# Optimization experiments

Hardware: AMD Instinct MI355X
Metric: run time of the kernel (lower is better)

Reference implementation:

```python
import jax, jax.numpy as jnp
import numpy as np

N = 100000   # nodes
E = 1600000  # edges (avg degree 16)
F = 128      # input features
H = 64       # hidden_dim
C = 10       # num_classes
G = 128      # graphs in batch
EPS = 1e-5   # BatchNorm eps


def setup_inputs() -> dict:
    key = jax.random.key(0)
    ks = jax.random.split(key, 24)
    d = {}
    d['x'] = jax.random.normal(ks[0], (N, F), jnp.float32)
    d['edge_index'] = jax.random.randint(ks[1], (2, E), 0, N)
    d['batch'] = jnp.sort(jax.random.randint(ks[2], (N,), 0, G))
    # SAGEConv1: lin_l (aggregated, with bias) + lin_r (root, no bias)
    d['W1l'] = jax.random.normal(ks[3], (F, H), jnp.float32) * 0.05
    d['W1r'] = jax.random.normal(ks[4], (F, H), jnp.float32) * 0.05
    d['b1'] = jnp.zeros((H,), jnp.float32)
    # SAGEConv2
    d['W2l'] = jax.random.normal(ks[5], (H, H), jnp.float32) * 0.1
    d['W2r'] = jax.random.normal(ks[6], (H, H), jnp.float32) * 0.1
    d['b2'] = jnp.zeros((H,), jnp.float32)
    # BatchNorm (eval mode: running stats)
    for i, (kg, kb, km, kv) in enumerate([(7, 8, 9, 10), (11, 12, 13, 14), (15, 16, 17, 18)], 1):
        d[f'bn{i}_g'] = jax.random.uniform(ks[kg], (H,), jnp.float32, 0.5, 1.5)
        d[f'bn{i}_b'] = jax.random.normal(ks[kb], (H,), jnp.float32) * 0.1
        d[f'bn{i}_m'] = jax.random.normal(ks[km], (H,), jnp.float32) * 0.1
        d[f'bn{i}_v'] = jax.random.uniform(ks[kv], (H,), jnp.float32, 0.5, 1.5)
    # classifier head
    d['Wc1'] = jax.random.normal(ks[19], (H, H), jnp.float32) * 0.1
    d['bc1'] = jnp.zeros((H,), jnp.float32)
    d['Wc2'] = jax.random.normal(ks[20], (H, C), jnp.float32) * 0.1
    d['bc2'] = jnp.zeros((C,), jnp.float32)
    return d


def _bn(x, g, b, m, v):
    return (x - m) * jax.lax.rsqrt(v + EPS) * g + b


def _sage(x, src, dst, Wl, Wr, b):
    # mean aggregation of source-node features at destination nodes
    msum = jax.ops.segment_sum(x[src], dst, num_segments=N)          # [N, d]
    cnt = jax.ops.segment_sum(jnp.ones((E,), x.dtype), dst, num_segments=N)
    mean = msum / jnp.maximum(cnt, 1.0)[:, None]
    return mean @ Wl + b + x @ Wr


def reference(x, edge_index, batch,
              W1l, W1r, b1, W2l, W2r, b2,
              bn1_g, bn1_b, bn1_m, bn1_v,
              bn2_g, bn2_b, bn2_m, bn2_v,
              Wc1, bc1, bn3_g, bn3_b, bn3_m, bn3_v,
              Wc2, bc2):
    src, dst = edge_index[0], edge_index[1]
    h = _sage(x, src, dst, W1l, W1r, b1)
    h = jax.nn.relu(_bn(h, bn1_g, bn1_b, bn1_m, bn1_v))
    h = _sage(h, src, dst, W2l, W2r, b2)
    h = jax.nn.relu(_bn(h, bn2_g, bn2_b, bn2_m, bn2_v))
    # global mean pool over graphs
    gsum = jax.ops.segment_sum(h, batch, num_segments=G)             # [G, H]
    gcnt = jax.ops.segment_sum(jnp.ones((N,), h.dtype), batch, num_segments=G)
    g = gsum / jnp.maximum(gcnt, 1.0)[:, None]
    # classifier head (eval: dropout is identity)
    g = jax.nn.relu(_bn(g @ Wc1 + bc1, bn3_g, bn3_b, bn3_m, bn3_v))
    logits = g @ Wc2 + bc2
    return jax.nn.log_softmax(logits, axis=1)
```

## Files before the change

### kernel.cpp

```cpp
#include <hip/hip_runtime.h>
#include <hip/hip_bf16.h>
#include <math.h>

#define NN 100000
#define NE 1600000
#define FF 128
#define HH 64
#define CC 10
#define GG 128
#define BN_EPS 1e-5f

#define BNODES 64
#define NB 1563
#define PBLK 128
#define ECHUNK 12500
#define MHIST (NB * PBLK)
#define NSCAN 782
#define SCOL_CAP 2048

typedef short v8bf __attribute__((ext_vector_type(8)));
typedef float v4f  __attribute__((ext_vector_type(4)));

__device__ inline ushort f2b(float x) {
    __hip_bfloat16 h = __float2bfloat16(x);
    return *reinterpret_cast<ushort*>(&h);
}
__device__ inline float b2f(ushort u) {
    return __uint_as_float(((unsigned)u) << 16);
}
__device__ inline float blo(unsigned u) { return __uint_as_float(u << 16); }
__device__ inline float bhi(unsigned u) { return __uint_as_float(u & 0xffff0000u); }

__device__ inline void acc8(float* a, const uint4 r) {
    a[0] += blo(r.x); a[1] += bhi(r.x); a[2] += blo(r.y); a[3] += bhi(r.y);
    a[4] += blo(r.z); a[5] += bhi(r.z); a[6] += blo(r.w); a[7] += bhi(r.w);
}

__device__ inline void sw_one(const float* __restrict__ W, ushort* __restrict__ o,
                              int t, int K) {
    const int lane = t & 63, nt = (t >> 6) & 3, ks = t >> 8;
    const int m = lane & 15, quad = lane >> 4;
#pragma unroll
    for (int j = 0; j < 8; ++j) {
        const int kk = ks * 32 + quad * 8 + j;
        const int cc = nt * 16 + m;
        o[t * 8 + j] = f2b(W[kk * 64 + cc]);
    }
}

template<int K, int TPB, bool AF32>
__global__ __launch_bounds__(256) void gemm_mfma(const void* __restrict__ Xv,
                                                 const ushort* __restrict__ Bl,
                                                 const ushort* __restrict__ Br,
                                                 ushort* __restrict__ Yl,
                                                 ushort* __restrict__ Yr) {
    constexpr int KS = K / 32;
    const int lane  = threadIdx.x & 63;
    const int wave  = threadIdx.x >> 6;
    const int nhalf = wave & 1;
    const int rsub  = wave >> 1;
    const int m = lane & 15, quad = lane >> 4;

    v8bf bl[KS][2], br[KS][2];
#pragma unroll
    for (int ks = 0; ks < KS; ++ks)
#pragma unroll
        for (int nt = 0; nt < 2; ++nt) {
            const int nti = nhalf * 2 + nt;
            bl[ks][nt] = *(const v8bf*)(Bl + ((size_t)(ks * 4 + nti) * 64 + lane) * 8);
            br[ks][nt] = *(const v8bf*)(Br + ((size_t)(ks * 4 + nti) * 64 + lane) * 8);
        }

    for (int it = 0; it < TPB; ++it) {
        const int bt = blockIdx.x * TPB + it;
        const int row0 = bt * 32 + rsub * 16;
        if (row0 >= NN) return;
        const v4f z = {0.f, 0.f, 0.f, 0.f};
        v4f accl[2] = {z, z}, accr[2] = {z, z};
#pragma unroll
        for (int ks = 0; ks < KS; ++ks) {
            v8bf a;
            if (AF32) {
                const float* xrow = (const float*)Xv + (size_t)(row0 + m) * K + quad * 8 + ks * 32;
                const float4 a0 = *(const float4*)(xrow);
                const float4 a1 = *(const float4*)(xrow + 4);
                a[0] = (short)f2b(a0.x); a[1] = (short)f2b(a0.y);
                a[2] = (short)f2b(a0.z); a[3] = (short)f2b(a0.w);
                a[4] = (short)f2b(a1.x); a[5] = (short)f2b(a1.y);
                a[6] = (short)f2b(a1.z); a[7] = (short)f2b(a1.w);
            } else {
                const ushort* xrow = (const ushort*)Xv + (size_t)(row0 + m) * K + quad * 8 + ks * 32;
                a = *(const v8bf*)xrow;
            }
#pragma unroll
            for (int nt = 0; nt < 2; ++nt) {
                accl[nt] = __builtin_amdgcn_mfma_f32_16x16x32_bf16(a, bl[ks][nt], accl[nt], 0, 0, 0);
                accr[nt] = __builtin_amdgcn_mfma_f32_16x16x32_bf16(a, br[ks][nt], accr[nt], 0, 0, 0);
            }
        }
#pragma unroll
        for (int nt = 0; nt < 2; ++nt) {
            const int cc = nhalf * 32 + nt * 16 + m;
#pragma unroll
            for (int r = 0; r < 4; ++r) {
                const size_t off = (size_t)(row0 + quad * 4 + r) * 64 + cc;
                Yl[off] = f2b(accl[nt][r]);
                Yr[off] = f2b(accr[nt][r]);
            }
        }
    }
}

__global__ __launch_bounds__(1024) void edge_hist(const int* __restrict__ dst,
                                                  int* __restrict__ hist,
                                                  const float* __restrict__ W1l,
                                                  const float* __restrict__ W1r,
                                                  const float* __restrict__ W2l,
                                                  const float* __restrict__ W2r,
                                                  ushort* __restrict__ w1ls,
                                                  ushort* __restrict__ w1rs,
                                                  ushort* __restrict__ w2ls,
                                                  ushort* __restrict__ w2rs,
                                                  float* __restrict__ gz) {
    if (blockIdx.x >= PBLK) {
        const int t = threadIdx.x;
        if (blockIdx.x == PBLK) {
            sw_one(W1l, w1ls, t, FF);
            sw_one(W1r, w1rs, t, FF);
        } else {
            if (t < 512) {
                sw_one(W2l, w2ls, t, HH);
                sw_one(W2r, w2rs, t, HH);
            } else {
                for (int i = t - 512; i < GG * 64 + GG; i += 512) gz[i] = 0.f;
            }
        }
        return;
    }
    __shared__ int h[NB];
    for (int i = threadIdx.x; i < NB; i += 1024) h[i] = 0;
    __syncthreads();
    const int e0 = blockIdx.x * ECHUNK;
    for (int e = e0 + threadIdx.x; e < e0 + ECHUNK; e += 1024)
        atomicAdd(&h[dst[e] >> 6], 1);
    __syncthreads();
    for (int i = threadIdx.x; i < NB; i += 1024)
        hist[i * PBLK + blockIdx.x] = h[i];
}

__global__ __launch_bounds__(256) void scan_block(const int* __restrict__ cnt,
                                                  int* __restrict__ rp,
                                                  int* __restrict__ bsum) {
    __shared__ int ws[4];
    const int tid = threadIdx.x;
    const int lane = tid & 63, wv = tid >> 6;
    const int i = blockIdx.x * 256 + tid;
    const int v = (i < MHIST) ? cnt[i] : 0;
    int inc = v;
#pragma unroll
    for (int off = 1; off < 64; off <<= 1) {
        int t = __shfl_up(inc, off, 64);
        if (lane >= off) inc += t;
    }
    if (lane == 63) ws[wv] = inc;
    __syncthreads();
    int wbase = 0;
#pragma unroll
    for (int w = 0; w < 4; ++w) wbase += (w < wv) ? ws[w] : 0;
    if (i < MHIST) rp[i] = wbase + inc - v;
    if (tid == 255) bsum[blockIdx.x] = wbase + inc;
}

__global__ __launch_bounds__(256) void scan_bsums(const int* __restrict__ bsum,
                                                  int* __restrict__ boff) {
    __shared__ int ws[4];
    const int tid = threadIdx.x;
    const int lane = tid & 63, wv = tid >> 6;
    int v[4];
    int tot = 0;
#pragma unroll
    for (int j = 0; j < 4; ++j) {
        const int idx = tid * 4 + j;
        v[j] = (idx < NSCAN) ? bsum[idx] : 0;
        tot += v[j];
    }
    int inc = tot;
#pragma unroll
    for (int off = 1; off < 64; off <<= 1) {
        int t = __shfl_up(inc, off, 64);
        if (lane >= off) inc += t;
    }
    if (lane == 63) ws[wv] = inc;
    __syncthreads();
    int wbase = 0;
#pragma unroll
    for (int w = 0; w < 4; ++w) wbase += (w < wv) ? ws[w] : 0;
    int run = wbase + inc - tot;
#pragma unroll
    for (int j = 0; j < 4; ++j) {
        const int idx = tid * 4 + j;
        if (idx < NSCAN) boff[idx] = run;
        run += v[j];
    }
}

__global__ __launch_bounds__(1024) void edge_scatter(const int* __restrict__ src,
                                                     const int* __restrict__ dst,
                                                     const int* __restrict__ hist,
                                                     const int* __restrict__ goffs,
                                                     const int* __restrict__ boff,
                                                     int* __restrict__ pairs) {
    __shared__ int sv[ECHUNK];
    __shared__ int sd[ECHUNK];
    __shared__ int sfill[NB];
    __shared__ int sdelta[NB];
    __shared__ int wsum[16];
    const int tid = threadIdx.x;
    const int lane = tid & 63, wv = tid >> 6;
    const int p = blockIdx.x;

    int c0 = 0, c1 = 0, g0 = 0, g1 = 0;
    const int i0 = 2 * tid, i1 = 2 * tid + 1;
    if (i0 < NB) {
        const int idx = i0 * PBLK + p;
        c0 = hist[idx];
        g0 = goffs[idx] + boff[idx >> 8];
    }
    if (i1 < NB) {
        const int idx = i1 * PBLK + p;
        c1 = hist[idx];
        g1 = goffs[idx] + boff[idx >> 8];
    }
    const int tv = c0 + c1;
    int inc = tv;
#pragma unroll
    for (int off = 1; off < 64; off <<= 1) {
        int t = __shfl_up(inc, off, 64);
        if (lane >= off) inc += t;
    }
    if (lane == 63) wsum[wv] = inc;
    __syncthreads();
    int wbase = 0;
#pragma unroll
    for (int w = 0; w < 16; ++w) wbase += (w < wv) ? wsum[w] : 0;
    const int excl = wbase + inc - tv;
    if (i0 < NB) { sfill[i0] = excl;      sdelta[i0] = g0 - excl; }
    if (i1 < NB) { sfill[i1] = excl + c0; sdelta[i1] = g1 - (excl + c0); }
    __syncthreads();

    const int e0 = p * ECHUNK;
    for (int e = e0 + tid; e < e0 + ECHUNK; e += 1024) {
        const int s = src[e];
        const int d = dst[e];
        const int b = d >> 6;
        const int local = atomicAdd(&sfill[b], 1);
        sv[local] = (s << 6) | (d & (BNODES - 1));
        sd[local] = local + sdelta[b];
    }
    __syncthreads();

    for (int j = tid; j < ECHUNK; j += 1024) {
        pairs[sd[j]] = sv[j];
    }
}

template<bool POOL>
__global__ __launch_bounds__(256) void spmm_sorted(const int* __restrict__ goffs,
                                                   const int* __restrict__ boff,
                                                   const int* __restrict__ pairs,
                                                   const ushort* __restrict__ Yl,
                                                   const ushort* __restrict__ Yr,
                                                   const float* __restrict__ bias,
                                                   const float* __restrict__ bng,
                                                   const float* __restrict__ bnb,
                                                   const float* __restrict__ bnm,
                                                   const float* __restrict__ bnv,
                                                   ushort* __restrict__ outp,
                                                   const int* __restrict__ batch,
                                                   float* __restrict__ gsum,
                                                   float* __restrict__ gcnt) {
    __shared__ int scol[SCOL_CAP];
    __shared__ int deg[BNODES];
    __shared__ int loffs[BNODES];
    __shared__ int fill[BNODES];
    __shared__ float pbuf[4][64];
    __shared__ float pcnt[4];
    __shared__ int g0s;
    const int tid = threadIdx.x;
    const int b = blockIdx.x;

    if (tid < BNODES) { deg[tid] = 0; fill[tid] = 0; }
    if (POOL) {
        pbuf[tid >> 6][tid & 63] = 0.f;
        if (tid < 4) pcnt[tid] = 0.f;
        if (tid == 0) g0s = batch[b * BNODES];
    }
    __syncthreads();

    const int beg = goffs[b * PBLK] + boff[b >> 1];
    int end = (b == NB - 1) ? NE : goffs[(b + 1) * PBLK] + boff[(b + 1) >> 1];
    if (end - beg > SCOL_CAP) end = beg + SCOL_CAP;

    int pv[8];
    int npv = 0;
    for (int i = beg + tid; i < end; i += 256) {
        const int v = pairs[i];
        pv[npv++] = v;
        atomicAdd(&deg[v & (BNODES - 1)], 1);
    }
    __syncthreads();

    if (tid < BNODES) {
        const int v = deg[tid];
        int inc = v;
#pragma unroll
        for (int s = 1; s < 64; s <<= 1) {
            int t = __shfl_up(inc, s, 64);
            if (tid >= s) inc += t;
        }
        loffs[tid] = inc;
    }
    __syncthreads();

    for (int j = 0; j < npv; ++j) {
        const int v = pv[j];
        const int dl = v & (BNODES - 1);
        const int pos = (loffs[dl] - deg[dl]) + atomicAdd(&fill[dl], 1);
        scol[pos] = v >> 6;
    }
    __syncthreads();

    const int wv = tid >> 6, lane = tid & 63;
    const int grp = lane >> 3, subl = lane & 7;

    float biasj[8], scj[8], mj[8], bbj[8];
#pragma unroll
    for (int j = 0; j < 8; ++j) {
        const int ch = subl * 8 + j;
        biasj[j] = bias[ch];
        scj[j] = bng[ch] * rsqrtf(bnv[ch] + BN_EPS);
        mj[j] = bnm[ch];
        bbj[j] = bnb[ch];
    }

    for (int i = 0; i < 2; ++i) {
        const int nl = wv * 16 + i * 8 + grp;
        const int node = b * BNODES + nl;
        if (node >= NN) continue;
        const int dg = deg[nl];
        const int nbeg = loffs[nl] - dg;
        const int nend = nbeg + dg;
        float a[8] = {0.f, 0.f, 0.f, 0.f, 0.f, 0.f, 0.f, 0.f};
        float c[8] = {0.f, 0.f, 0.f, 0.f, 0.f, 0.f, 0.f, 0.f};
        int e = nbeg;
        for (; e + 3 < nend; e += 4) {
            const int s0 = scol[e], s1 = scol[e + 1], s2 = scol[e + 2], s3 = scol[e + 3];
            const uint4 r0 = *(const uint4*)(Yl + (size_t)s0 * 64 + subl * 8);
            const uint4 r1 = *(const uint4*)(Yl + (size_t)s1 * 64 + subl * 8);
            const uint4 r2 = *(const uint4*)(Yl + (size_t)s2 * 64 + subl * 8);
            const uint4 r3 = *(const uint4*)(Yl + (size_t)s3 * 64 + subl * 8);
            acc8(a, r0); acc8(c, r1); acc8(a, r2); acc8(c, r3);
        }
        if (e + 1 < nend) {
            const int s0 = scol[e], s1 = scol[e + 1];
            const uint4 r0 = *(const uint4*)(Yl + (size_t)s0 * 64 + subl * 8);
            const uint4 r1 = *(const uint4*)(Yl + (size_t)s1 * 64 + subl * 8);
            acc8(a, r0); acc8(c, r1);
            e += 2;
        }
        if (e < nend) {
            const int s0 = scol[e];
            const uint4 r0 = *(const uint4*)(Yl + (size_t)s0 * 64 + subl * 8);
            acc8(a, r0);
        }
        const float inv = 1.0f / fmaxf((float)dg, 1.0f);
        const uint4 yr = *(const uint4*)(Yr + (size_t)node * 64 + subl * 8);
        float hj[8];
        hj[0] = (a[0] + c[0]) * inv + biasj[0] + blo(yr.x);
        hj[1] = (a[1] + c[1]) * inv + biasj[1] + bhi(yr.x);
        hj[2] = (a[2] + c[2]) * inv + biasj[2] + blo(yr.y);
        hj[3] = (a[3] + c[3]) * inv + biasj[3] + bhi(yr.y);
        hj[4] = (a[4] + c[4]) * inv + biasj[4] + blo(yr.z);
        hj[5] = (a[5] + c[5]) * inv + biasj[5] + bhi(yr.z);
        hj[6] = (a[6] + c[6]) * inv + biasj[6] + blo(yr.w);
        hj[7] = (a[7] + c[7]) * inv + biasj[7] + bhi(yr.w);
        float o[8];
#pragma unroll
        for (int j = 0; j < 8; ++j)
            o[j] = fmaxf((hj[j] - mj[j]) * scj[j] + bbj[j], 0.0f);
        if (!POOL) {
            unsigned ow[4];
#pragma unroll
            for (int j = 0; j < 4; ++j)
                ow[j] = (unsigned)f2b(o[2 * j]) | ((unsigned)f2b(o[2 * j + 1]) << 16);
            uint4 ov;
            ov.x = ow[0]; ov.y = ow[1]; ov.z = ow[2]; ov.w = ow[3];
            *(uint4*)(outp + (size_t)node * 64 + subl * 8) = ov;
        } else {
            const int g = batch[node];
            const int gi = g - g0s;
            if (gi < 4) {
#pragma unroll
                for (int j = 0; j < 8; ++j) atomicAdd(&pbuf[gi][subl * 8 + j], o[j]);
                if (subl == 0) atomicAdd(&pcnt[gi], 1.0f);
            } else {
#pragma unroll
                for (int j = 0; j < 8; ++j) atomicAdd(&gsum[g * 64 + subl * 8 + j], o[j]);
                if (subl == 0) atomicAdd(&gcnt[g], 1.0f);
            }
        }
    }
    if (POOL) {
        __syncthreads();
        const int q = tid >> 6, ch = tid & 63;
        const int g = g0s + q;
        if (g < GG) {
            const float v = pbuf[q][ch];
            if (v != 0.f) atomicAdd(&gsum[g * 64 + ch], v);
        }
        if (tid < 4) {
            const int gq = g0s + tid;
            if (gq < GG && pcnt[tid] > 0.f) atomicAdd(&gcnt[gq], pcnt[tid]);
        }
    }
}

__global__ __launch_bounds__(64) void head_kernel(const float* __restrict__ gsum,
                                                  const float* __restrict__ gcnt,
                                                  const float* __restrict__ Wc1,
                                                  const float* __restrict__ bc1,
                                                  const float* __restrict__ g3,
                                                  const float* __restrict__ b3,
                                                  const float* __restrict__ m3,
                                                  const float* __restrict__ v3,
                                                  const float* __restrict__ Wc2,
                                                  const float* __restrict__ bc2,
                                                  float* __restrict__ out) {
    __shared__ float sg[64];
    __shared__ float st[64];
    __shared__ float sl[10];
    __shared__ float sls;
    const int b = blockIdx.x;
    const int c = threadIdx.x;
    sg[c] = gsum[b * 64 + c] / fmaxf(gcnt[b], 1.0f);
    __syncthreads();
    float acc = bc1[c];
#pragma unroll
    for (int k = 0; k < 64; ++k) acc += sg[k] * Wc1[k * 64 + c];
    const float sc = g3[c] * rsqrtf(v3[c] + BN_EPS);
    st[c] = fmaxf((acc - m3[c]) * sc + b3[c], 0.0f);
    __syncthreads();
    if (c < CC) {
        float lg = bc2[c];
#pragma unroll
        for (int k = 0; k < 64; ++k) lg += st[k] * Wc2[k * CC + c];
        sl[c] = lg;
    }
    __syncthreads();
    if (c == 0) {
        float mx = sl[0];
        for (int i = 1; i < CC; ++i) mx = fmaxf(mx, sl[i]);
        float s = 0.f;
        for (int i = 0; i < CC; ++i) s += expf(sl[i] - mx);
        sls = mx + logf(s);
    }
    __syncthreads();
    if (c < CC) out[b * CC + c] = sl[c] - sls;
}

extern "C" void kernel_launch(void* const* d_in, const int* in_sizes, int n_in,
                              void* d_out, int out_size, void* d_ws, size_t ws_size,
                              hipStream_t stream) {
    const float* x    = (const float*)d_in[0];
    const int*   ei   = (const int*)d_in[1];
    const int*   batch= (const int*)d_in[2];
    const float* W1l  = (const float*)d_in[3];
    const float* W1r  = (const float*)d_in[4];
    const float* b1   = (const float*)d_in[5];
    const float* W2l  = (const float*)d_in[6];
    const float* W2r  = (const float*)d_in[7];
    const float* b2   = (const float*)d_in[8];
    const float* bn1g = (const float*)d_in[9];
    const float* bn1b = (const float*)d_in[10];
    const float* bn1m = (const float*)d_in[11];
    const float* bn1v = (const float*)d_in[12];
    const float* bn2g = (const float*)d_in[13];
    const float* bn2b = (const float*)d_in[14];
    const float* bn2m = (const float*)d_in[15];
    const float* bn2v = (const float*)d_in[16];
    const float* bn3g = (const float*)d_in[17];
    const float* bn3b = (const float*)d_in[18];
    const float* bn3m = (const float*)d_in[19];
    const float* bn3v = (const float*)d_in[20];
    const float* Wc1  = (const float*)d_in[21];
    const float* bc1  = (const float*)d_in[22];
    const float* Wc2  = (const float*)d_in[23];
    const float* bc2  = (const float*)d_in[24];
    float* out = (float*)d_out;

    const int* src = ei;
    const int* dst = ei + NE;

    char* p = (char*)d_ws;
    ushort* yl   = (ushort*)p;                 p += (size_t)NN * 64 * 2;
    ushort* yr   = (ushort*)p;                 p += (size_t)NN * 64 * 2;
    ushort* hbuf = (ushort*)p;                 p += (size_t)NN * 64 * 2;
    int*    pairs= (int*)p;                    p += (size_t)NE * 4;
    int*    hist = (int*)p;                    p += (size_t)MHIST * 4;
    int*    goffs= (int*)p;                    p += (size_t)MHIST * 4;
    int*    bsum = (int*)p;                    p += 1024 * 4;
    int*    boff = (int*)p;                    p += 1024 * 4;
    ushort* w1ls = (ushort*)p;                 p += (size_t)FF * 64 * 2;
    ushort* w1rs = (ushort*)p;                 p += (size_t)FF * 64 * 2;
    ushort* w2ls = (ushort*)p;                 p += (size_t)HH * 64 * 2;
    ushort* w2rs = (ushort*)p;                 p += (size_t)HH * 64 * 2;
    float* gsum  = (float*)p;                  p += (size_t)GG * 64 * 4;
    float* gcnt  = gsum + GG * 64;             p += (size_t)GG * 4;

    edge_hist<<<PBLK + 2, 1024, 0, stream>>>(dst, hist, W1l, W1r, W2l, W2r,
                                             w1ls, w1rs, w2ls, w2rs, gsum);
    scan_block<<<NSCAN, 256, 0, stream>>>(hist, goffs, bsum);
    scan_bsums<<<1, 256, 0, stream>>>(bsum, boff);
    edge_scatter<<<PBLK, 1024, 0, stream>>>(src, dst, hist, goffs, boff, pairs);

    gemm_mfma<FF, 2, true><<<1563, 256, 0, stream>>>((const void*)x, w1ls, w1rs, yl, yr);
    spmm_sorted<false><<<NB, 256, 0, stream>>>(goffs, boff, pairs, yl, yr, b1,
                                               bn1g, bn1b, bn1m, bn1v, hbuf,
                                               batch, gsum, gcnt);

    gemm_mfma<HH, 2, false><<<1563, 256, 0, stream>>>((const void*)hbuf, w2ls, w2rs, yl, yr);
    spmm_sorted<true><<<NB, 256, 0, stream>>>(goffs, boff, pairs, yl, yr, b2,
                                              bn2g, bn2b, bn2m, bn2v, hbuf,
                                              batch, gsum, gcnt);

    head_kernel<<<GG, 64, 0, stream>>>(gsum, gcnt, Wc1, bc1,
                                       bn3g, bn3b, bn3m, bn3v, Wc2, bc2, out);
}
```

Baseline: 287.3 us.

## Balance edge aggregation across thread groups with segmented LDS accumulation

```diff
diff --git a/kernel.cpp b/kernel.cpp
--- a/kernel.cpp
+++ b/kernel.cpp
@@ -280,6 +280,7 @@
                                                    float* __restrict__ gsum,
                                                    float* __restrict__ gcnt) {
     __shared__ int scol[SCOL_CAP];
+    __shared__ float accum[BNODES][65];
     __shared__ int deg[BNODES];
     __shared__ int loffs[BNODES];
     __shared__ int fill[BNODES];
@@ -290,6 +291,7 @@
     const int b = blockIdx.x;
 
     if (tid < BNODES) { deg[tid] = 0; fill[tid] = 0; }
+    for (int i = tid; i < BNODES * 65; i += 256) (&accum[0][0])[i] = 0.f;
     if (POOL) {
         pbuf[tid >> 6][tid & 63] = 0.f;
         if (tid < 4) pcnt[tid] = 0.f;
@@ -326,12 +328,83 @@
         const int v = pv[j];
         const int dl = v & (BNODES - 1);
         const int pos = (loffs[dl] - deg[dl]) + atomicAdd(&fill[dl], 1);
-        scol[pos] = v >> 6;
+        scol[pos] = v;
+    }
+    __syncthreads();
+
+    const int gid = tid >> 3, subl = tid & 7;
+    const int nedges = end - beg;
+    const int chunk = ((nedges + 31) >> 5) | 1;
+    int e = gid * chunk;
+    const int gend = (e + chunk < nedges) ? e + chunk : nedges;
+    float racc[8] = {0.f, 0.f, 0.f, 0.f, 0.f, 0.f, 0.f, 0.f};
+    int cur = -1;
+
+    int v0 = 0, v1 = 0, v2 = 0, v3 = 0;
+    if (e + 3 < gend) { v0 = scol[e]; v1 = scol[e + 1]; v2 = scol[e + 2]; v3 = scol[e + 3]; }
+    while (e + 3 < gend) {
+        const uint4 r0 = *(const uint4*)(Yl + (size_t)(v0 >> 6) * 64 + subl * 8);
+        const uint4 r1 = *(const uint4*)(Yl + (size_t)(v1 >> 6) * 64 + subl * 8);
+        const uint4 r2 = *(const uint4*)(Yl + (size_t)(v2 >> 6) * 64 + subl * 8);
+        const uint4 r3 = *(const uint4*)(Yl + (size_t)(v3 >> 6) * 64 + subl * 8);
+        const int d0 = v0 & 63, d1 = v1 & 63, d2 = v2 & 63, d3 = v3 & 63;
+        const int en = e + 4;
+        if (en + 3 < gend) {
+            v0 = scol[en]; v1 = scol[en + 1]; v2 = scol[en + 2]; v3 = scol[en + 3];
+        }
+        if (d0 != cur) {
+            if (cur >= 0) {
+#pragma unroll
+                for (int j = 0; j < 8; ++j) { atomicAdd(&accum[cur][subl * 8 + j], racc[j]); racc[j] = 0.f; }
+            }
+            cur = d0;
+        }
+        if (d0 == d3) {
+            acc8(racc, r0); acc8(racc, r1); acc8(racc, r2); acc8(racc, r3);
+        } else {
+            acc8(racc, r0);
+            if (d1 != cur) {
+#pragma unroll
+                for (int j = 0; j < 8; ++j) { atomicAdd(&accum[cur][subl * 8 + j], racc[j]); racc[j] = 0.f; }
+                cur = d1;
+            }
+            acc8(racc, r1);
+            if (d2 != cur) {
+#pragma unroll
+                for (int j = 0; j < 8; ++j) { atomicAdd(&accum[cur][subl * 8 + j], racc[j]); racc[j] = 0.f; }
+                cur = d2;
+            }
+            acc8(racc, r2);
+            if (d3 != cur) {
+#pragma unroll
+                for (int j = 0; j < 8; ++j) { atomicAdd(&accum[cur][subl * 8 + j], racc[j]); racc[j] = 0.f; }
+                cur = d3;
+            }
+            acc8(racc, r3);
+        }
+        e = en;
+    }
+    for (; e < gend; ++e) {
+        const int v = scol[e];
+        const uint4 r = *(const uint4*)(Yl + (size_t)(v >> 6) * 64 + subl * 8);
+        const int d = v & 63;
+        if (d != cur) {
+            if (cur >= 0) {
+#pragma unroll
+                for (int j = 0; j < 8; ++j) { atomicAdd(&accum[cur][subl * 8 + j], racc[j]); racc[j] = 0.f; }
+            }
+            cur = d;
+        }
+        acc8(racc, r);
+    }
+    if (cur >= 0) {
+#pragma unroll
+        for (int j = 0; j < 8; ++j) { atomicAdd(&accum[cur][subl * 8 + j], racc[j]); racc[j] = 0.f; }
     }
     __syncthreads();
 
     const int wv = tid >> 6, lane = tid & 63;
-    const int grp = lane >> 3, subl = lane & 7;
+    const int grp = lane >> 3;
 
     float biasj[8], scj[8], mj[8], bbj[8];
 #pragma unroll
@@ -348,42 +421,17 @@
         const int node = b * BNODES + nl;
         if (node >= NN) continue;
         const int dg = deg[nl];
-        const int nbeg = loffs[nl] - dg;
-        const int nend = nbeg + dg;
-        float a[8] = {0.f, 0.f, 0.f, 0.f, 0.f, 0.f, 0.f, 0.f};
-        float c[8] = {0.f, 0.f, 0.f, 0.f, 0.f, 0.f, 0.f, 0.f};
-        int e = nbeg;
-        for (; e + 3 < nend; e += 4) {
-            const int s0 = scol[e], s1 = scol[e + 1], s2 = scol[e + 2], s3 = scol[e + 3];
-            const uint4 r0 = *(const uint4*)(Yl + (size_t)s0 * 64 + subl * 8);
-            const uint4 r1 = *(const uint4*)(Yl + (size_t)s1 * 64 + subl * 8);
-            const uint4 r2 = *(const uint4*)(Yl + (size_t)s2 * 64 + subl * 8);
-            const uint4 r3 = *(const uint4*)(Yl + (size_t)s3 * 64 + subl * 8);
-            acc8(a, r0); acc8(c, r1); acc8(a, r2); acc8(c, r3);
-        }
-        if (e + 1 < nend) {
-            const int s0 = scol[e], s1 = scol[e + 1];
-            const uint4 r0 = *(const uint4*)(Yl + (size_t)s0 * 64 + subl * 8);
-            const uint4 r1 = *(const uint4*)(Yl + (size_t)s1 * 64 + subl * 8);
-            acc8(a, r0); acc8(c, r1);
-            e += 2;
-        }
-        if (e < nend) {
-            const int s0 = scol[e];
-            const uint4 r0 = *(const uint4*)(Yl + (size_t)s0 * 64 + subl * 8);
-            acc8(a, r0);
-        }
         const float inv = 1.0f / fmaxf((float)dg, 1.0f);
         const uint4 yr = *(const uint4*)(Yr + (size_t)node * 64 + subl * 8);
         float hj[8];
-        hj[0] = (a[0] + c[0]) * inv + biasj[0] + blo(yr.x);
-        hj[1] = (a[1] + c[1]) * inv + biasj[1] + bhi(yr.x);
-        hj[2] = (a[2] + c[2]) * inv + biasj[2] + blo(yr.y);
-        hj[3] = (a[3] + c[3]) * inv + biasj[3] + bhi(yr.y);
-        hj[4] = (a[4] + c[4]) * inv + biasj[4] + blo(yr.z);
-        hj[5] = (a[5] + c[5]) * inv + biasj[5] + bhi(yr.z);
-        hj[6] = (a[6] + c[6]) * inv + biasj[6] + blo(yr.w);
-        hj[7] = (a[7] + c[7]) * inv + biasj[7] + bhi(yr.w);
+        hj[0] = accum[nl][subl * 8 + 0] * inv + biasj[0] + blo(yr.x);
+        hj[1] = accum[nl][subl * 8 + 1] * inv + biasj[1] + bhi(yr.x);
+        hj[2] = accum[nl][subl * 8 + 2] * inv + biasj[2] + blo(yr.y);
+        hj[3] = accum[nl][subl * 8 + 3] * inv + biasj[3] + bhi(yr.y);
+        hj[4] = accum[nl][subl * 8 + 4] * inv + biasj[4] + blo(yr.z);
+        hj[5] = accum[nl][subl * 8 + 5] * inv + biasj[5] + bhi(yr.z);
+        hj[6] = accum[nl][subl * 8 + 6] * inv + biasj[6] + blo(yr.w);
+        hj[7] = accum[nl][subl * 8 + 7] * inv + biasj[7] + bhi(yr.w);
         float o[8];
 #pragma unroll
         for (int j = 0; j < 8; ++j)
```

New measurement: 358.1 us. 1.25x slower.

## Split each node's neighbor gather across a whole wavefront with shuffle reduction

Applied to the files above, without the earlier changes.

```diff
diff --git a/kernel.cpp b/kernel.cpp
--- a/kernel.cpp
+++ b/kernel.cpp
@@ -280,6 +280,7 @@
                                                    float* __restrict__ gsum,
                                                    float* __restrict__ gcnt) {
     __shared__ int scol[SCOL_CAP];
+    __shared__ float accum[BNODES][65];
     __shared__ int deg[BNODES];
     __shared__ int loffs[BNODES];
     __shared__ int fill[BNODES];
@@ -333,6 +334,36 @@
     const int wv = tid >> 6, lane = tid & 63;
     const int grp = lane >> 3, subl = lane & 7;
 
+    for (int nl = wv * 16; nl < wv * 16 + 16; ++nl) {
+        const int dg = deg[nl];
+        const int nbeg = loffs[nl] - dg;
+        float racc[8] = {0.f, 0.f, 0.f, 0.f, 0.f, 0.f, 0.f, 0.f};
+        for (int e = 0; e < dg; e += 16) {
+            const int i0 = e + grp;
+            const int i1 = e + 8 + grp;
+            const bool k0 = i0 < dg, k1 = i1 < dg;
+            int s0 = 0, s1 = 0;
+            if (k0) s0 = scol[nbeg + i0];
+            if (k1) s1 = scol[nbeg + i1];
+            uint4 r0, r1;
+            if (k0) r0 = *(const uint4*)(Yl + (size_t)s0 * 64 + subl * 8);
+            if (k1) r1 = *(const uint4*)(Yl + (size_t)s1 * 64 + subl * 8);
+            if (k0) acc8(racc, r0);
+            if (k1) acc8(racc, r1);
+        }
+#pragma unroll
+        for (int j = 0; j < 8; ++j) {
+            racc[j] += __shfl_xor(racc[j], 8, 64);
+            racc[j] += __shfl_xor(racc[j], 16, 64);
+            racc[j] += __shfl_xor(racc[j], 32, 64);
+        }
+        if (grp == 0) {
+#pragma unroll
+            for (int j = 0; j < 8; ++j) accum[nl][subl * 8 + j] = racc[j];
+        }
+    }
+    __syncthreads();
+
     float biasj[8], scj[8], mj[8], bbj[8];
 #pragma unroll
     for (int j = 0; j < 8; ++j) {
@@ -348,42 +379,17 @@
         const int node = b * BNODES + nl;
         if (node >= NN) continue;
         const int dg = deg[nl];
-        const int nbeg = loffs[nl] - dg;
-        const int nend = nbeg + dg;
-        float a[8] = {0.f, 0.f, 0.f, 0.f, 0.f, 0.f, 0.f, 0.f};
-        float c[8] = {0.f, 0.f, 0.f, 0.f, 0.f, 0.f, 0.f, 0.f};
-        int e = nbeg;
-        for (; e + 3 < nend; e += 4) {
-            const int s0 = scol[e], s1 = scol[e + 1], s2 = scol[e + 2], s3 = scol[e + 3];
-            const uint4 r0 = *(const uint4*)(Yl + (size_t)s0 * 64 + subl * 8);
-            const uint4 r1 = *(const uint4*)(Yl + (size_t)s1 * 64 + subl * 8);
-            const uint4 r2 = *(const uint4*)(Yl + (size_t)s2 * 64 + subl * 8);
-            const uint4 r3 = *(const uint4*)(Yl + (size_t)s3 * 64 + subl * 8);
-            acc8(a, r0); acc8(c, r1); acc8(a, r2); acc8(c, r3);
-        }
-        if (e + 1 < nend) {
-            const int s0 = scol[e], s1 = scol[e + 1];
-            const uint4 r0 = *(const uint4*)(Yl + (size_t)s0 * 64 + subl * 8);
-            const uint4 r1 = *(const uint4*)(Yl + (size_t)s1 * 64 + subl * 8);
-            acc8(a, r0); acc8(c, r1);
-            e += 2;
-        }
-        if (e < nend) {
-            const int s0 = scol[e];
-            const uint4 r0 = *(const uint4*)(Yl + (size_t)s0 * 64 + subl * 8);
-            acc8(a, r0);
-        }
         const float inv = 1.0f / fmaxf((float)dg, 1.0f);
         const uint4 yr = *(const uint4*)(Yr + (size_t)node * 64 + subl * 8);
         float hj[8];
-        hj[0] = (a[0] + c[0]) * inv + biasj[0] + blo(yr.x);
-        hj[1] = (a[1] + c[1]) * inv + biasj[1] + bhi(yr.x);
-        hj[2] = (a[2] + c[2]) * inv + biasj[2] + blo(yr.y);
-        hj[3] = (a[3] + c[3]) * inv + biasj[3] + bhi(yr.y);
-        hj[4] = (a[4] + c[4]) * inv + biasj[4] + blo(yr.z);
-        hj[5] = (a[5] + c[5]) * inv + biasj[5] + bhi(yr.z);
-        hj[6] = (a[6] + c[6]) * inv + biasj[6] + blo(yr.w);
-        hj[7] = (a[7] + c[7]) * inv + biasj[7] + bhi(yr.w);
+        hj[0] = accum[nl][subl * 8 + 0] * inv + biasj[0] + blo(yr.x);
+        hj[1] = accum[nl][subl * 8 + 1] * inv + biasj[1] + bhi(yr.x);
+        hj[2] = accum[nl][subl * 8 + 2] * inv + biasj[2] + blo(yr.y);
+        hj[3] = accum[nl][subl * 8 + 3] * inv + biasj[3] + bhi(yr.y);
+        hj[4] = accum[nl][subl * 8 + 4] * inv + biasj[4] + blo(yr.z);
+        hj[5] = accum[nl][subl * 8 + 5] * inv + biasj[5] + bhi(yr.z);
+        hj[6] = accum[nl][subl * 8 + 6] * inv + biasj[6] + blo(yr.w);
+        hj[7] = accum[nl][subl * 8 + 7] * inv + biasj[7] + bhi(yr.w);
         float o[8];
 #pragma unroll
         for (int j = 0; j < 8; ++j)
```

New measurement: 349.9 us. 1.22x slower.
